# Optimization experiments

Measured on AMD Instinct MI355X. Metric: run time of the kernel, lower is better.

Reference implementation:

```python
import jax, jax.numpy as jnp
import numpy as np

DIM = 768
NUM_HEADS = 16
HEAD_DIM = DIM // NUM_HEADS  # 48


def setup_inputs() -> dict:
    key = jax.random.key(0)
    ks = jax.random.split(key, 9)
    s = 1.0 / np.sqrt(DIM)
    return {
        "x": jax.random.normal(ks[0], (4, 2048, DIM), dtype=jnp.float32),
        "Wq": jax.random.uniform(ks[1], (DIM, DIM), jnp.float32, -s, s),
        "bq": jax.random.uniform(ks[2], (DIM,), jnp.float32, -s, s),
        "Wk": jax.random.uniform(ks[3], (DIM, DIM), jnp.float32, -s, s),
        "bk": jax.random.uniform(ks[4], (DIM,), jnp.float32, -s, s),
        "Wv": jax.random.uniform(ks[5], (DIM, DIM), jnp.float32, -s, s),
        "bv": jax.random.uniform(ks[6], (DIM,), jnp.float32, -s, s),
        "Wo": jax.random.uniform(ks[7], (DIM, DIM), jnp.float32, -s, s),
        "bo": jax.random.uniform(ks[8], (DIM,), jnp.float32, -s, s),
    }


def reference(x, Wq, bq, Wk, bk, Wv, bv, Wo, bo):
    B, S, D = x.shape
    H, Dh = NUM_HEADS, HEAD_DIM
    # qkv projections -> [B, H, S, Dh]
    q = (x @ Wq.T + bq).reshape(B, S, H, Dh).transpose(0, 2, 1, 3)
    k = (x @ Wk.T + bk).reshape(B, S, H, Dh).transpose(0, 2, 1, 3)
    v = (x @ Wv.T + bv).reshape(B, S, H, Dh).transpose(0, 2, 1, 3)
    scale = 1.0 / np.sqrt(Dh).astype(np.float32)
    scores = jnp.einsum('bhqd,bhkd->bhqk', q, k) * scale  # [B,H,S,S]
    attn = jax.nn.softmax(scores, axis=-1)
    # dropout is identity in eval mode
    out = jnp.einsum('bhqk,bhkd->bhqd', attn, v)  # [B,H,S,Dh]
    out = out.transpose(0, 2, 1, 3).reshape(B, S, D)
    return out @ Wo.T + bo
```

## Files before the change

kernel.cpp:

```cpp
#include <hip/hip_runtime.h>
#include <cstdint>
#include <cstddef>


typedef short s8v __attribute__((ext_vector_type(8)));
typedef float f4v __attribute__((ext_vector_type(4)));

static constexpr int Bn = 4, Sn = 2048, Dn = 768, Hn = 16, DhN = 48, Dp = 64;
static constexpr int MS = Bn * Sn;

#define MFMA16(a, b, c) __builtin_amdgcn_mfma_f32_16x16x32_bf16((a), (b), (c), 0, 0, 0)

__device__ __forceinline__ ushort f2b(float f) {
  return (ushort)((__builtin_bit_cast(uint32_t, f) + 0x8000u) >> 16);
}
__device__ __forceinline__ uint32_t packbf(float a, float b) {
  uint32_t ua = (__builtin_bit_cast(uint32_t, a) + 0x8000u) >> 16;
  uint32_t ub = (__builtin_bit_cast(uint32_t, b) + 0x8000u) & 0xffff0000u;
  return ua | ub;
}
__device__ __forceinline__ float fexp2(float x) {
  return __builtin_amdgcn_exp2f(x);
}
__device__ __forceinline__ void gload_lds16(const ushort* g, ushort* l) {
  __builtin_amdgcn_global_load_lds(
      (const __attribute__((address_space(1))) uint32_t*)g,
      (__attribute__((address_space(3))) uint32_t*)l, 16, 0, 0);
}

__global__ void cvt_kernel(const float* __restrict__ src, ushort* __restrict__ dst, int n4) {
  int i = blockIdx.x * blockDim.x + threadIdx.x;
  if (i < n4) {
    float4 f = ((const float4*)src)[i];
    ushort4 o = { f2b(f.x), f2b(f.y), f2b(f.z), f2b(f.w) };
    ((ushort4*)dst)[i] = o;
  }
}

__global__ void cvt_w_kernel(const float* __restrict__ wq, const float* __restrict__ wk,
                             const float* __restrict__ wv, const float* __restrict__ wo,
                             ushort* __restrict__ dqkv, ushort* __restrict__ dо_unused,
                             ushort* __restrict__ dо) {
  const int region = blockIdx.x / 576;
  const int i = (blockIdx.x % 576) * 256 + threadIdx.x;
  const float* src = (region == 0) ? wq : (region == 1) ? wk : (region == 2) ? wv : wo;
  ushort* dst = (region < 3) ? (dqkv + (size_t)region * Dn * Dn) : dо;
  float4 f = ((const float4*)src)[i];
  ushort4 o = { f2b(f.x), f2b(f.y), f2b(f.z), f2b(f.w) };
  ((ushort4*)dst)[i] = o;
}

__global__ __launch_bounds__(256) void gemm_qkv(
    const ushort* __restrict__ A, const ushort* __restrict__ W,
    const float* __restrict__ bq, const float* __restrict__ bk, const float* __restrict__ bv,
    ushort* __restrict__ outq, ushort* __restrict__ outk, ushort* __restrict__ outv,
    float qscale) {
  __shared__ __align__(16) ushort As[128][32];
  __shared__ __align__(16) ushort Bs[128][32];
  const int tid = threadIdx.x, lane = tid & 63, wave = tid >> 6;
  const int l15 = lane & 15, g = lane >> 4;
  const int m0 = blockIdx.y * 128, n0 = blockIdx.x * 128;
  const int wqm = (wave >> 1) * 64;
  const int wqx = (wave & 1) * 64;
  f4v acc[4][4] = {};

  const int slot0 = wave * 128 + lane;
  const int slot1 = slot0 + 64;
  const int r0 = slot0 >> 2, u0 = (slot0 & 3) * 8;
  const int r1 = slot1 >> 2, u1 = (slot1 & 3) * 8;
  const ushort* ag0 = A + (size_t)(m0 + r0) * Dn + u0;
  const ushort* ag1 = A + (size_t)(m0 + r1) * Dn + u1;
  const ushort* bg0 = W + (size_t)(n0 + r0) * Dn + u0;
  const ushort* bg1 = W + (size_t)(n0 + r1) * Dn + u1;
  ushort* lA0 = &As[0][0] + slot0 * 8;
  ushort* lA1 = &As[0][0] + slot1 * 8;
  ushort* lB0 = &Bs[0][0] + slot0 * 8;
  ushort* lB1 = &Bs[0][0] + slot1 * 8;

  for (int k0 = 0; k0 < Dn; k0 += 32) {
    __syncthreads();
    gload_lds16(ag0 + k0, lA0);
    gload_lds16(ag1 + k0, lA1);
    gload_lds16(bg0 + k0, lB0);
    gload_lds16(bg1 + k0, lB1);
    __syncthreads();
    s8v wf[4], xf[4];
#pragma unroll
    for (int i = 0; i < 4; ++i) wf[i] = *(const s8v*)&Bs[wqm + i * 16 + l15][g * 8];
#pragma unroll
    for (int j = 0; j < 4; ++j) xf[j] = *(const s8v*)&As[wqx + j * 16 + l15][g * 8];
#pragma unroll
    for (int i = 0; i < 4; ++i)
#pragma unroll
      for (int j = 0; j < 4; ++j) acc[i][j] = MFMA16(wf[i], xf[j], acc[i][j]);
  }

  const int region = blockIdx.x / 6;
  const int nbase = n0 - region * 768;
  const float* bias = (region == 0) ? bq : (region == 1) ? bk : bv;
#pragma unroll
  for (int i = 0; i < 4; ++i) {
    const int n = nbase + wqm + i * 16 + g * 4;
    const float4 b4 = *(const float4*)&bias[n];
    const int h = n / DhN, dh = n - h * DhN;
#pragma unroll
    for (int j = 0; j < 4; ++j) {
      const int s = m0 + wqx + j * 16 + l15;
      const int b = s >> 11, srow = s & 2047;
      const int bh = b * Hn + h;
      float v0 = acc[i][j][0] + b4.x, v1 = acc[i][j][1] + b4.y;
      float v2 = acc[i][j][2] + b4.z, v3 = acc[i][j][3] + b4.w;
      if (region == 0) { v0 *= qscale; v1 *= qscale; v2 *= qscale; v3 *= qscale; }
      if (region < 2) {
        ushort4 o = { f2b(v0), f2b(v1), f2b(v2), f2b(v3) };
        ushort* dst = region ? outk : outq;
        *(ushort4*)&dst[((size_t)bh * Sn + srow) * Dp + dh] = o;
      } else {
        outv[((size_t)bh * DhN + dh + 0) * Sn + srow] = f2b(v0);
        outv[((size_t)bh * DhN + dh + 1) * Sn + srow] = f2b(v1);
        outv[((size_t)bh * DhN + dh + 2) * Sn + srow] = f2b(v2);
        outv[((size_t)bh * DhN + dh + 3) * Sn + srow] = f2b(v3);
      }
    }
  }
}

__global__ __launch_bounds__(256) void gemm_out(
    const ushort* __restrict__ A, const ushort* __restrict__ W,
    const float* __restrict__ bias, float* __restrict__ out) {
  __shared__ __align__(16) ushort As[128][32];
  __shared__ __align__(16) ushort Bs[128][32];
  const int tid = threadIdx.x, lane = tid & 63, wave = tid >> 6;
  const int l15 = lane & 15, g = lane >> 4;
  const int m0 = blockIdx.y * 128, n0 = blockIdx.x * 128;
  const int wqm = (wave >> 1) * 64;
  const int wqx = (wave & 1) * 64;
  f4v acc[4][4] = {};

  const int slot0 = wave * 128 + lane;
  const int slot1 = slot0 + 64;
  const int r0 = slot0 >> 2, u0 = (slot0 & 3) * 8;
  const int r1 = slot1 >> 2, u1 = (slot1 & 3) * 8;
  const ushort* ag0 = A + (size_t)(m0 + r0) * Dn + u0;
  const ushort* ag1 = A + (size_t)(m0 + r1) * Dn + u1;
  const ushort* bg0 = W + (size_t)(n0 + r0) * Dn + u0;
  const ushort* bg1 = W + (size_t)(n0 + r1) * Dn + u1;
  ushort* lA0 = &As[0][0] + slot0 * 8;
  ushort* lA1 = &As[0][0] + slot1 * 8;
  ushort* lB0 = &Bs[0][0] + slot0 * 8;
  ushort* lB1 = &Bs[0][0] + slot1 * 8;

  for (int k0 = 0; k0 < Dn; k0 += 32) {
    __syncthreads();
    gload_lds16(ag0 + k0, lA0);
    gload_lds16(ag1 + k0, lA1);
    gload_lds16(bg0 + k0, lB0);
    gload_lds16(bg1 + k0, lB1);
    __syncthreads();
    s8v wf[4], xf[4];
#pragma unroll
    for (int i = 0; i < 4; ++i) wf[i] = *(const s8v*)&Bs[wqm + i * 16 + l15][g * 8];
#pragma unroll
    for (int j = 0; j < 4; ++j) xf[j] = *(const s8v*)&As[wqx + j * 16 + l15][g * 8];
#pragma unroll
    for (int i = 0; i < 4; ++i)
#pragma unroll
      for (int j = 0; j < 4; ++j) acc[i][j] = MFMA16(wf[i], xf[j], acc[i][j]);
  }

#pragma unroll
  for (int i = 0; i < 4; ++i) {
    const int n = n0 + wqm + i * 16 + g * 4;
    const float4 b4 = *(const float4*)&bias[n];
#pragma unroll
    for (int j = 0; j < 4; ++j) {
      const int s = m0 + wqx + j * 16 + l15;
      float4 o4 = { acc[i][j][0] + b4.x, acc[i][j][1] + b4.y,
                    acc[i][j][2] + b4.z, acc[i][j][3] + b4.w };
      *(float4*)&out[(size_t)s * Dn + n] = o4;
    }
  }
}

__global__ __launch_bounds__(128) void attn_kernel(
    const ushort* __restrict__ qg, const ushort* __restrict__ kg,
    const ushort* __restrict__ vg, ushort* __restrict__ og) {
  __shared__ __align__(16) ushort Ks[2][64][32];
  __shared__ __align__(16) ushort Vs[2][64][32];
  __shared__ __align__(16) ushort Ps[2][64][48];
  const int tid = threadIdx.x;
  const int lane = tid & 63;
  const int wave = tid >> 6;
  const int l15 = lane & 15;
  const int g = lane >> 4;
  const int bh = blockIdx.y;
  const int q0 = blockIdx.x * 128;
  const ushort* qb = qg + (size_t)bh * Sn * Dp;
  const ushort* kb = kg + (size_t)bh * Sn * Dp;
  const ushort* vb = vg + (size_t)bh * DhN * Sn;

  {
#pragma unroll
    for (int t = 0; t < 4; ++t) {
      const int idx = tid * 4 + t;
      const int half = idx >> 8;
      const int rem = idx & 255;
      const int row = 48 + (rem >> 4);
      const int col = (rem & 15) * 2;
      *(uint32_t*)&Vs[half][row][col] = (row == 48) ? 0x3F803F80u : 0u;
    }
  }

  s8v qa[4][2];
#pragma unroll
  for (int nt = 0; nt < 4; ++nt)
#pragma unroll
    for (int kc = 0; kc < 2; ++kc)
      qa[nt][kc] = *(const s8v*)(qb + (size_t)(q0 + wave * 64 + nt * 16 + l15) * Dp + kc * 32 + g * 8);

  const ushort* gsrc[7];
  ushort* ldst[7];
  int gstep[7];
#pragma unroll
  for (int t = 0; t < 7; ++t) {
    const int c = wave + 2 * t;
    if (c < 8) {
      const int half = c >> 2, rr = (c & 3) * 16;
      gsrc[t] = kb + (size_t)(rr + (lane >> 2)) * Dp + half * 32 + (lane & 3) * 8;
      ldst[t] = &Ks[half][rr][0] + lane * 8;
      gstep[t] = 64 * Dp;
    } else {
      const int cc = c - 8;
      const int half = cc >= 3 ? 1 : 0;
      const int rr = (cc - half * 3) * 16;
      gsrc[t] = vb + (size_t)(rr + (lane >> 2)) * Sn + half * 32 + (lane & 3) * 8;
      ldst[t] = &Vs[half][rr][0] + lane * 8;
      gstep[t] = 64;
    }
  }

  f4v acc[4][4] = {};

  for (int kt = 0; kt < Sn; kt += 64) {
    __syncthreads();
#pragma unroll
    for (int t = 0; t < 7; ++t) {
      gload_lds16(gsrc[t], ldst[t]);
      gsrc[t] += gstep[t];
    }
    __syncthreads();

#pragma unroll
    for (int half = 0; half < 2; ++half) {
#pragma unroll
      for (int lmt = 0; lmt < 2; ++lmt) {
        const int mt = half * 2 + lmt;
        s8v ka0 = *(const s8v*)&Ks[0][mt * 16 + l15][g * 8];
        s8v ka1 = *(const s8v*)&Ks[1][mt * 16 + l15][g * 8];
#pragma unroll
        for (int nt = 0; nt < 4; ++nt) {
          f4v z = {};
          z = MFMA16(ka0, qa[nt][0], z);
          f4v st = MFMA16(ka1, qa[nt][1], z);
          const float p0 = fexp2(st[0]), p1 = fexp2(st[1]);
          const float p2 = fexp2(st[2]), p3 = fexp2(st[3]);
          uint2 pw;
          pw.x = packbf(p0, p1);
          pw.y = packbf(p2, p3);
          *(uint2*)&Ps[wave][nt * 16 + l15][lmt * 16 + g * 4] = pw;
        }
      }
      s8v vf[4];
#pragma unroll
      for (int d = 0; d < 4; ++d) vf[d] = *(const s8v*)&Vs[half][d * 16 + l15][g * 8];
#pragma unroll
      for (int nt = 0; nt < 4; ++nt) {
        s8v pa = *(const s8v*)&Ps[wave][nt * 16 + l15][g * 8];
#pragma unroll
        for (int d = 0; d < 4; ++d) acc[nt][d] = MFMA16(pa, vf[d], acc[nt][d]);
      }
    }
  }

  const int b = bh >> 4, h = bh & 15;
#pragma unroll
  for (int nt = 0; nt < 4; ++nt) {
#pragma unroll
    for (int r = 0; r < 4; ++r) {
      const float lq = __shfl(acc[nt][3][r], g * 16, 64);
      const float inv = 1.0f / lq;
      const int s = q0 + wave * 64 + nt * 16 + g * 4 + r;
      const size_t base = ((size_t)(b * Sn + s)) * Dn + h * DhN;
#pragma unroll
      for (int d = 0; d < 3; ++d)
        og[base + d * 16 + l15] = f2b(acc[nt][d][r] * inv);
    }
  }
}

extern "C" void kernel_launch(void* const* d_in, const int* in_sizes, int n_in,
                              void* d_out, int out_size, void* d_ws, size_t ws_size,
                              hipStream_t stream) {
  (void)in_sizes; (void)n_in; (void)out_size; (void)ws_size;
  const float* x  = (const float*)d_in[0];
  const float* Wq = (const float*)d_in[1];
  const float* bq = (const float*)d_in[2];
  const float* Wk = (const float*)d_in[3];
  const float* bk = (const float*)d_in[4];
  const float* Wv = (const float*)d_in[5];
  const float* bv = (const float*)d_in[6];
  const float* Wo = (const float*)d_in[7];
  const float* bo = (const float*)d_in[8];

  size_t off = 0;
  auto alloc = [&](size_t bytes) {
    void* p = (char*)d_ws + off;
    off += (bytes + 255) & ~(size_t)255;
    return p;
  };
  ushort* xb    = (ushort*)alloc((size_t)MS * Dn * 2);
  ushort* Wqkvb = (ushort*)alloc((size_t)3 * Dn * Dn * 2);
  ushort* Wob   = (ushort*)alloc((size_t)Dn * Dn * 2);
  ushort* qbuf  = (ushort*)alloc((size_t)Bn * Hn * Sn * Dp * 2);
  ushort* kbuf  = (ushort*)alloc((size_t)Bn * Hn * Sn * Dp * 2);
  ushort* vbuf  = (ushort*)alloc((size_t)Bn * Hn * DhN * Sn * 2);
  ushort* ao    = (ushort*)alloc((size_t)MS * Dn * 2);

  const int n4x = MS * Dn / 4;
  cvt_kernel<<<(n4x + 255) / 256, 256, 0, stream>>>(x, xb, n4x);
  cvt_w_kernel<<<4 * 576, 256, 0, stream>>>(Wq, Wk, Wv, Wo, Wqkvb, nullptr, Wob);

  hipMemsetAsync(qbuf, 0, (size_t)Bn * Hn * Sn * Dp * 2, stream);

  const dim3 blk(256);
  const float qscale = 0.20823510929813633f;
  gemm_qkv<<<dim3(18, MS / 128), blk, 0, stream>>>(xb, Wqkvb, bq, bk, bv,
                                                   qbuf, kbuf, vbuf, qscale);

  attn_kernel<<<dim3(Sn / 128, Bn * Hn), dim3(128), 0, stream>>>(qbuf, kbuf, vbuf, ao);

  gemm_out<<<dim3(6, MS / 128), blk, 0, stream>>>(ao, Wob, bo, (float*)d_out);
}
```

Before: 272.1 us.

## Merge conversion kernels, zero Q padding in GEMM epilogue, use 4-wave attention blocks

```diff
diff --git a/kernel.cpp b/kernel.cpp
--- a/kernel.cpp
+++ b/kernel.cpp
@@ -28,23 +28,23 @@
       (__attribute__((address_space(3))) uint32_t*)l, 16, 0, 0);
 }
 
-__global__ void cvt_kernel(const float* __restrict__ src, ushort* __restrict__ dst, int n4) {
-  int i = blockIdx.x * blockDim.x + threadIdx.x;
-  if (i < n4) {
-    float4 f = ((const float4*)src)[i];
-    ushort4 o = { f2b(f.x), f2b(f.y), f2b(f.z), f2b(f.w) };
-    ((ushort4*)dst)[i] = o;
-  }
-}
-
-__global__ void cvt_w_kernel(const float* __restrict__ wq, const float* __restrict__ wk,
-                             const float* __restrict__ wv, const float* __restrict__ wo,
-                             ushort* __restrict__ dqkv, ushort* __restrict__ dо_unused,
-                             ushort* __restrict__ dо) {
-  const int region = blockIdx.x / 576;
-  const int i = (blockIdx.x % 576) * 256 + threadIdx.x;
-  const float* src = (region == 0) ? wq : (region == 1) ? wk : (region == 2) ? wv : wo;
-  ushort* dst = (region < 3) ? (dqkv + (size_t)region * Dn * Dn) : dо;
+__global__ void cvt_all(const float* __restrict__ x,
+                        const float* __restrict__ wq, const float* __restrict__ wk,
+                        const float* __restrict__ wv, const float* __restrict__ wo,
+                        ushort* __restrict__ xb, ushort* __restrict__ wqkv,
+                        ushort* __restrict__ wob) {
+  const int bid = blockIdx.x;
+  const float* src;
+  ushort* dst;
+  int i;
+  if (bid < 6144) {
+    src = x; dst = xb; i = bid * 256 + threadIdx.x;
+  } else {
+    const int r = (bid - 6144) / 576;
+    i = ((bid - 6144) % 576) * 256 + threadIdx.x;
+    src = (r == 0) ? wq : (r == 1) ? wk : (r == 2) ? wv : wo;
+    dst = (r < 3) ? (wqkv + (size_t)r * Dn * Dn) : wob;
+  }
   float4 f = ((const float4*)src)[i];
   ushort4 o = { f2b(f.x), f2b(f.y), f2b(f.z), f2b(f.w) };
   ((ushort4*)dst)[i] = o;
@@ -114,7 +114,13 @@
       if (region < 2) {
         ushort4 o = { f2b(v0), f2b(v1), f2b(v2), f2b(v3) };
         ushort* dst = region ? outk : outq;
-        *(ushort4*)&dst[((size_t)bh * Sn + srow) * Dp + dh] = o;
+        const size_t base = ((size_t)bh * Sn + srow) * Dp;
+        *(ushort4*)&dst[base + dh] = o;
+        if (region == 0 && dh < 4) {
+          const uint4 z = {0, 0, 0, 0};
+          *(uint4*)&dst[base + 48] = z;
+          *(uint4*)&dst[base + 56] = z;
+        }
       } else {
         outv[((size_t)bh * DhN + dh + 0) * Sn + srow] = f2b(v0);
         outv[((size_t)bh * DhN + dh + 1) * Sn + srow] = f2b(v1);
@@ -182,12 +188,12 @@
   }
 }
 
-__global__ __launch_bounds__(128) void attn_kernel(
+__global__ __launch_bounds__(256) void attn_kernel(
     const ushort* __restrict__ qg, const ushort* __restrict__ kg,
     const ushort* __restrict__ vg, ushort* __restrict__ og) {
   __shared__ __align__(16) ushort Ks[2][64][32];
   __shared__ __align__(16) ushort Vs[2][64][32];
-  __shared__ __align__(16) ushort Ps[2][64][48];
+  __shared__ __align__(16) ushort Ps[4][32][48];
   const int tid = threadIdx.x;
   const int lane = tid & 63;
   const int wave = tid >> 6;
@@ -199,52 +205,52 @@
   const ushort* kb = kg + (size_t)bh * Sn * Dp;
   const ushort* vb = vg + (size_t)bh * DhN * Sn;
 
-  {
-#pragma unroll
-    for (int t = 0; t < 4; ++t) {
-      const int idx = tid * 4 + t;
-      const int half = idx >> 8;
-      const int rem = idx & 255;
-      const int row = 48 + (rem >> 4);
-      const int col = (rem & 15) * 2;
-      *(uint32_t*)&Vs[half][row][col] = (row == 48) ? 0x3F803F80u : 0u;
-    }
-  }
-
-  s8v qa[4][2];
-#pragma unroll
-  for (int nt = 0; nt < 4; ++nt)
+#pragma unroll
+  for (int t = 0; t < 2; ++t) {
+    const int idx = tid + t * 256;
+    const int half = idx >> 8;
+    const int rem = idx & 255;
+    const int row = 48 + (rem >> 4);
+    const int col = (rem & 15) * 2;
+    *(uint32_t*)&Vs[half][row][col] = (row == 48) ? 0x3F803F80u : 0u;
+  }
+
+  s8v qa[2][2];
+#pragma unroll
+  for (int nt = 0; nt < 2; ++nt)
 #pragma unroll
     for (int kc = 0; kc < 2; ++kc)
-      qa[nt][kc] = *(const s8v*)(qb + (size_t)(q0 + wave * 64 + nt * 16 + l15) * Dp + kc * 32 + g * 8);
-
-  const ushort* gsrc[7];
-  ushort* ldst[7];
-  int gstep[7];
-#pragma unroll
-  for (int t = 0; t < 7; ++t) {
-    const int c = wave + 2 * t;
+      qa[nt][kc] = *(const s8v*)(qb + (size_t)(q0 + wave * 32 + nt * 16 + l15) * Dp + kc * 32 + g * 8);
+
+  const ushort* gsrc[4];
+  ushort* ldst[4];
+  int gstep[4];
+  const int nchunk = (wave < 2) ? 4 : 3;
+#pragma unroll
+  for (int t = 0; t < 4; ++t) {
+    const int c = wave + 4 * t;
     if (c < 8) {
       const int half = c >> 2, rr = (c & 3) * 16;
       gsrc[t] = kb + (size_t)(rr + (lane >> 2)) * Dp + half * 32 + (lane & 3) * 8;
       ldst[t] = &Ks[half][rr][0] + lane * 8;
       gstep[t] = 64 * Dp;
-    } else {
+    } else if (c < 14) {
       const int cc = c - 8;
       const int half = cc >= 3 ? 1 : 0;
       const int rr = (cc - half * 3) * 16;
       gsrc[t] = vb + (size_t)(rr + (lane >> 2)) * Sn + half * 32 + (lane & 3) * 8;
       ldst[t] = &Vs[half][rr][0] + lane * 8;
       gstep[t] = 64;
-    }
-  }
-
-  f4v acc[4][4] = {};
+    } else {
+      gsrc[t] = nullptr; ldst[t] = nullptr; gstep[t] = 0;
+    }
+  }
+
+  f4v acc[2][4] = {};
 
   for (int kt = 0; kt < Sn; kt += 64) {
     __syncthreads();
-#pragma unroll
-    for (int t = 0; t < 7; ++t) {
+    for (int t = 0; t < nchunk; ++t) {
       gload_lds16(gsrc[t], ldst[t]);
       gsrc[t] += gstep[t];
     }
@@ -258,7 +264,7 @@
         s8v ka0 = *(const s8v*)&Ks[0][mt * 16 + l15][g * 8];
         s8v ka1 = *(const s8v*)&Ks[1][mt * 16 + l15][g * 8];
 #pragma unroll
-        for (int nt = 0; nt < 4; ++nt) {
+        for (int nt = 0; nt < 2; ++nt) {
           f4v z = {};
           z = MFMA16(ka0, qa[nt][0], z);
           f4v st = MFMA16(ka1, qa[nt][1], z);
@@ -274,7 +280,7 @@
 #pragma unroll
       for (int d = 0; d < 4; ++d) vf[d] = *(const s8v*)&Vs[half][d * 16 + l15][g * 8];
 #pragma unroll
-      for (int nt = 0; nt < 4; ++nt) {
+      for (int nt = 0; nt < 2; ++nt) {
         s8v pa = *(const s8v*)&Ps[wave][nt * 16 + l15][g * 8];
 #pragma unroll
         for (int d = 0; d < 4; ++d) acc[nt][d] = MFMA16(pa, vf[d], acc[nt][d]);
@@ -284,12 +290,12 @@
 
   const int b = bh >> 4, h = bh & 15;
 #pragma unroll
-  for (int nt = 0; nt < 4; ++nt) {
+  for (int nt = 0; nt < 2; ++nt) {
 #pragma unroll
     for (int r = 0; r < 4; ++r) {
       const float lq = __shfl(acc[nt][3][r], g * 16, 64);
       const float inv = 1.0f / lq;
-      const int s = q0 + wave * 64 + nt * 16 + g * 4 + r;
+      const int s = q0 + wave * 32 + nt * 16 + g * 4 + r;
       const size_t base = ((size_t)(b * Sn + s)) * Dn + h * DhN;
 #pragma unroll
       for (int d = 0; d < 3; ++d)
@@ -326,18 +332,14 @@
   ushort* vbuf  = (ushort*)alloc((size_t)Bn * Hn * DhN * Sn * 2);
   ushort* ao    = (ushort*)alloc((size_t)MS * Dn * 2);
 
-  const int n4x = MS * Dn / 4;
-  cvt_kernel<<<(n4x + 255) / 256, 256, 0, stream>>>(x, xb, n4x);
-  cvt_w_kernel<<<4 * 576, 256, 0, stream>>>(Wq, Wk, Wv, Wo, Wqkvb, nullptr, Wob);
-
-  hipMemsetAsync(qbuf, 0, (size_t)Bn * Hn * Sn * Dp * 2, stream);
+  cvt_all<<<6144 + 4 * 576, 256, 0, stream>>>(x, Wq, Wk, Wv, Wo, xb, Wqkvb, Wob);
 
   const dim3 blk(256);
   const float qscale = 0.20823510929813633f;
   gemm_qkv<<<dim3(18, MS / 128), blk, 0, stream>>>(xb, Wqkvb, bq, bk, bv,
                                                    qbuf, kbuf, vbuf, qscale);
 
-  attn_kernel<<<dim3(Sn / 128, Bn * Hn), dim3(128), 0, stream>>>(qbuf, kbuf, vbuf, ao);
+  attn_kernel<<<dim3(Sn / 128, Bn * Hn), blk, 0, stream>>>(qbuf, kbuf, vbuf, ao);
 
   gemm_out<<<dim3(6, MS / 128), blk, 0, stream>>>(ao, Wob, bo, (float*)d_out);
 }
```

Result: faster. 266.4 us (-2.1%).
